# Kernel tuning notes

Measured on AMD Instinct MI355X. Metric: run time of the kernel, lower is better.

## Reference

```python
import jax, jax.numpy as jnp
import numpy as np

DT_RANK = 160
D_STATE = 16


def setup_inputs() -> dict:
    key = jax.random.key(0)
    ks = jax.random.split(key, 13)
    B, D, E = 32, 2560, 5120
    s = lambda k, shape, sc=0.02: (jax.random.normal(k, shape, dtype=jnp.float32) * sc)
    return {
        "x": jax.random.normal(ks[0], (1, 1, B, D), dtype=jnp.float32),
        "W_in_ssm": s(ks[1], (D, E)),
        "W_in_mlp": s(ks[2], (D, E)),
        "W_out": s(ks[3], (E, D)),
        "conv_w": s(ks[4], (4, B, E), 0.1),
        "conv_b": s(ks[5], (B, E), 0.1),
        "conv_states": jax.random.normal(ks[6], (3, 1, 1, B, E), dtype=jnp.float32),
        "Wx": s(ks[7], (E, DT_RANK + 2 * D_STATE)),
        "W_dt": s(ks[8], (DT_RANK, E)),
        "dt_bias": s(ks[9], (E,), 0.5),
        "A_log": jax.random.uniform(ks[10], (E, D_STATE), dtype=jnp.float32),
        "D": s(ks[11], (E,), 1.0),
        "h": jax.random.normal(ks[12], (B, E, D_STATE), dtype=jnp.float32) * 0.1,
    }


def reference(x, W_in_ssm, W_in_mlp, W_out, conv_w, conv_b, conv_states, Wx, W_dt, dt_bias, A_log, D, h):
    # x: [1,1,B,d_model]
    x_ssm = x @ W_in_ssm  # [1,1,B,E]
    # FIFO: 3 carried conv states + newest projection -> 4 taps
    states = jnp.concatenate([conv_states, x_ssm[None]], axis=0)  # [4,1,1,B,E]
    # unrolled 4-tap causal depthwise conv (per-batch-broadcast weights) + bias + SiLU
    conv = jnp.einsum('tabne,tne->abne', states, conv_w) + conv_b  # [1,1,B,E]
    conv = jax.nn.silu(conv)

    # --- single-step selective SSM (Mamba decode) ---
    xt = conv[0, 0]  # [B,E]
    dbc = xt @ Wx  # [B, dt_rank + 2*d_state]
    dt = jax.nn.softplus(dbc[:, :DT_RANK] @ W_dt + dt_bias)  # [B,E]
    Bm = dbc[:, DT_RANK:DT_RANK + D_STATE]  # [B,N]
    Cm = dbc[:, DT_RANK + D_STATE:]         # [B,N]
    A = -jnp.exp(A_log)                      # [E,N]
    dA = jnp.exp(dt[:, :, None] * A[None])   # [B,E,N]
    h_new = h * dA + (dt[:, :, None] * Bm[:, None, :]) * xt[:, :, None]
    y = jnp.einsum('ben,bn->be', h_new, Cm) + D * xt  # [B,E]
    y = y[None, None]  # [1,1,B,E]

    # gated residual branch: silu-activated mlp projection
    residual = jax.nn.silu(x @ W_in_mlp)  # [1,1,B,E]
    out = y * residual
    return out @ W_out  # [1,1,B,d_model]
```

## Files before the change

kernel.cpp:

```cpp
#include <hip/hip_runtime.h>
#include <math.h>

#define EE 5120
#define DD 2560
#define BB 32

typedef __attribute__((ext_vector_type(8)))  short  short8;
typedef __attribute__((ext_vector_type(8)))  __bf16 bf16x8;
typedef __attribute__((ext_vector_type(16))) float  f32x16;

__device__ __forceinline__ void split8(const float* v, short8& hi, short8& lo) {
#pragma unroll
  for (int j = 0; j < 8; ++j) {
    unsigned u = __float_as_uint(v[j]);
    hi[j] = (short)(u >> 16);
    float r = v[j] - __uint_as_float(u & 0xFFFF0000u);
    lo[j] = (short)(__float_as_uint(r) >> 16);
  }
}
#define BC(x) __builtin_bit_cast(bf16x8, x)

__device__ __forceinline__ void g2l16(const float* g, float* l) {
  __builtin_amdgcn_global_load_lds(
      (const __attribute__((address_space(1))) void*)g,
      (__attribute__((address_space(3))) void*)l, 16, 0, 0);
}

__global__ __launch_bounds__(256) void k0_prep(const float* __restrict__ x,
                                               float* __restrict__ xT,
                                               float* __restrict__ dbc) {
  int g = blockIdx.x * 256 + threadIdx.x;
  if (g < BB * DD) {
    int b = g / DD, k = g % DD;
    xT[k * BB + b] = x[g];
  }
  if (g < BB * 192) dbc[g] = 0.f;
}

__global__ __launch_bounds__(256) void gemm_mfma(const float* __restrict__ W0,
                                                 const float* __restrict__ W1,
                                                 int wsplit, int wstride,
                                                 const float* __restrict__ xsrc,
                                                 float* __restrict__ P,
                                                 int pstride, int ncb) {
  __shared__ float red[4 * 64 * 17];
  const int cb   = blockIdx.x % ncb;
  const int so   = blockIdx.x / ncb;
  const int lane = threadIdx.x & 63;
  const int wv   = __builtin_amdgcn_readfirstlane((int)(threadIdx.x >> 6));
  const int c0   = cb * 64;
  const float* __restrict__ W = (c0 < wsplit) ? W0 : W1;
  const int wc0  = (c0 < wsplit) ? c0 : c0 - wsplit;
  const int kw   = so * 320 + wv * 80;
  const int kl   = (lane >> 5) * 8;
  const int ln   = lane & 31;

  float av[5][8];
#pragma unroll
  for (int s = 0; s < 5; ++s)
#pragma unroll
    for (int j = 0; j < 8; ++j)
      av[s][j] = xsrc[(size_t)(kw + s * 16 + kl + j) * BB + ln];
  short8 ah[5], al[5];
#pragma unroll
  for (int s = 0; s < 5; ++s) split8(av[s], ah[s], al[s]);

#pragma unroll
  for (int t = 0; t < 2; ++t) {
    f32x16 acc;
#pragma unroll
    for (int i = 0; i < 16; ++i) acc[i] = 0.f;

    const float* __restrict__ wp =
        W + (size_t)kw * wstride + wc0 + t * 32 + ln;

    float bv0[8], bv1[8];
#pragma unroll
    for (int j = 0; j < 8; ++j) bv0[j] = wp[(size_t)(kl + j) * wstride];
#pragma unroll
    for (int s = 0; s < 5; ++s) {
      float (&cur)[8] = (s & 1) ? bv1 : bv0;
      float (&nxt)[8] = (s & 1) ? bv0 : bv1;
      if (s < 4) {
#pragma unroll
        for (int j = 0; j < 8; ++j)
          nxt[j] = wp[(size_t)((s + 1) * 16 + kl + j) * wstride];
      }
      short8 bh, bl;
      split8(cur, bh, bl);
      acc = __builtin_amdgcn_mfma_f32_32x32x16_bf16(BC(ah[s]), BC(bh), acc, 0, 0, 0);
      acc = __builtin_amdgcn_mfma_f32_32x32x16_bf16(BC(al[s]), BC(bh), acc, 0, 0, 0);
      acc = __builtin_amdgcn_mfma_f32_32x32x16_bf16(BC(ah[s]), BC(bl), acc, 0, 0, 0);
    }

    __syncthreads();
#pragma unroll
    for (int r = 0; r < 16; ++r) red[(wv * 64 + lane) * 17 + r] = acc[r];
    __syncthreads();
#pragma unroll
    for (int q = 0; q < 4; ++q) {
      int r = wv * 4 + q;
      float sum = red[(0 * 64 + lane) * 17 + r] + red[(1 * 64 + lane) * 17 + r] +
                  red[(2 * 64 + lane) * 17 + r] + red[(3 * 64 + lane) * 17 + r];
      int row = (r & 3) + 8 * (r >> 2) + 4 * (lane >> 5);
      P[((size_t)(so * 32 + row)) * pstride + c0 + t * 32 + ln] = sum;
    }
  }
}

__global__ __launch_bounds__(256) void k1b_epilogue(const float* __restrict__ P1,
                                                    const float* __restrict__ cs,
                                                    const float* __restrict__ cw,
                                                    const float* __restrict__ cbv,
                                                    float* __restrict__ xt,
                                                    float* __restrict__ res) {
  int g = blockIdx.x * 256 + threadIdx.x;
  int e = g % EE;
  int b = g / EE;
  float xs = 0.f, xm = 0.f;
#pragma unroll
  for (int so = 0; so < 8; ++so) {
    xs += P1[((size_t)(so * BB + b)) * 10240 + e];
    xm += P1[((size_t)(so * BB + b)) * 10240 + EE + e];
  }
  size_t be = (size_t)b * EE + e;
  const size_t T = (size_t)BB * EE;
  float conv = cs[be] * cw[be] + cs[T + be] * cw[T + be] +
               cs[2 * T + be] * cw[2 * T + be] + xs * cw[3 * T + be] + cbv[be];
  float sig = 1.f / (1.f + expf(-conv));
  xt[be] = conv * sig;
  float sm = 1.f / (1.f + expf(-xm));
  res[be] = xm * sm;
}

__global__ __launch_bounds__(256) void k2_dbc(const float* __restrict__ xt,
                                              const float* __restrict__ Wx,
                                              float* __restrict__ dbc) {
  const int bid  = blockIdx.x;
  const int cbi  = bid % 3;
  const int so   = bid / 3;
  const int lane = threadIdx.x & 63;
  const int j    = cbi * 64 + lane;
  const int k0   = so * 80 + (int)(threadIdx.x >> 6) * 20;

  float acc[BB];
#pragma unroll
  for (int b = 0; b < BB; ++b) acc[b] = 0.f;

  for (int kk = 0; kk < 20; kk += 4) {
    int k = k0 + kk;
    float w0 = Wx[(size_t)(k + 0) * 192 + j];
    float w1 = Wx[(size_t)(k + 1) * 192 + j];
    float w2 = Wx[(size_t)(k + 2) * 192 + j];
    float w3 = Wx[(size_t)(k + 3) * 192 + j];
#pragma unroll
    for (int b = 0; b < BB; ++b) acc[b] = fmaf(xt[(size_t)b * EE + k + 0], w0, acc[b]);
#pragma unroll
    for (int b = 0; b < BB; ++b) acc[b] = fmaf(xt[(size_t)b * EE + k + 1], w1, acc[b]);
#pragma unroll
    for (int b = 0; b < BB; ++b) acc[b] = fmaf(xt[(size_t)b * EE + k + 2], w2, acc[b]);
#pragma unroll
    for (int b = 0; b < BB; ++b) acc[b] = fmaf(xt[(size_t)b * EE + k + 3], w3, acc[b]);
  }

  __shared__ float red2[4][64][17];
  const int ksid = threadIdx.x >> 6;
#pragma unroll
  for (int half = 0; half < 2; ++half) {
    __syncthreads();
#pragma unroll
    for (int i = 0; i < 16; ++i) red2[ksid][lane][i] = acc[half * 16 + i];
    __syncthreads();
#pragma unroll
    for (int jj = 0; jj < 4; ++jj) {
      int bi = ksid * 4 + jj;
      float v = red2[0][lane][bi] + red2[1][lane][bi] +
                red2[2][lane][bi] + red2[3][lane][bi];
      int b = half * 16 + bi;
      atomicAdd(&dbc[b * 192 + j], v);
    }
  }
}

__global__ __launch_bounds__(256) void k3_ssm(const float* __restrict__ dbc,
                                              const float* __restrict__ Wdt,
                                              const float* __restrict__ dt_bias,
                                              const float* __restrict__ A_log,
                                              const float* __restrict__ Dvec,
                                              const float* __restrict__ h,
                                              const float* __restrict__ xt,
                                              const float* __restrict__ res,
                                              float* __restrict__ zT) {
  __shared__ float sw[10240];
  const int eb   = blockIdx.x % 80;
  const int bg   = blockIdx.x / 80;
  const int lane = threadIdx.x & 63;
  const int wv   = __builtin_amdgcn_readfirstlane((int)(threadIdx.x >> 6));
  const int e    = eb * 64 + lane;
  const int bq   = bg * 4 + wv;
  const int b0   = bq * 2, b1 = b0 + 1;

  {
    const int rg = lane >> 4, cg = (lane & 15) * 4;
#pragma unroll
    for (int j = 0; j < 10; ++j) {
      int r = wv * 40 + j * 4 + rg;
      g2l16(Wdt + (size_t)r * EE + eb * 64 + cg, sw + (wv * 40 + j * 4) * 64);
    }
  }
  __syncthreads();

  float a0 = 0.f, a1 = 0.f;
  const float* __restrict__ d0 = dbc + b0 * 192;
  const float* __restrict__ d1 = dbc + b1 * 192;
#pragma unroll 4
  for (int r = 0; r < 160; ++r) {
    float w = sw[r * 64 + lane];
    a0 = fmaf(d0[r], w, a0);
    a1 = fmaf(d1[r], w, a1);
  }

  float An[16];
#pragma unroll
  for (int n = 0; n < 16; ++n) An[n] = -expf(A_log[e * 16 + n]);
  const float bias = dt_bias[e];
  const float Dv = Dvec[e];

#pragma unroll
  for (int t = 0; t < 2; ++t) {
    int b = t ? b1 : b0;
    float a = t ? a1 : a0;
    float v = a + bias;
    float dt = (v > 20.f) ? v : log1pf(expf(v));
    size_t be = (size_t)b * EE + e;
    float xb = xt[be];
    const float* __restrict__ hb = h + be * 16;
    const float* __restrict__ Bm = dbc + b * 192 + 160;
    const float* __restrict__ Cm = dbc + b * 192 + 176;
    float y = 0.f;
#pragma unroll
    for (int n = 0; n < 16; ++n) {
      float dA = expf(dt * An[n]);
      float hn = fmaf(hb[n], dA, dt * Bm[n] * xb);
      y = fmaf(hn, Cm[n], y);
    }
    y = fmaf(Dv, xb, y);
    zT[e * BB + b] = y * res[be];
  }
}

__global__ __launch_bounds__(256) void k4b_reduce(const float* __restrict__ P4,
                                                  float* __restrict__ out) {
  int g = blockIdx.x * 256 + threadIdx.x;
  int d = g % DD;
  int b = g / DD;
  float s = 0.f;
#pragma unroll
  for (int so = 0; so < 16; ++so) s += P4[((size_t)(so * BB + b)) * DD + d];
  out[g] = s;
}

extern "C" void kernel_launch(void* const* d_in, const int* in_sizes, int n_in,
                              void* d_out, int out_size, void* d_ws, size_t ws_size,
                              hipStream_t stream) {
  const float* x       = (const float*)d_in[0];
  const float* Wssm    = (const float*)d_in[1];
  const float* Wmlp    = (const float*)d_in[2];
  const float* Wout    = (const float*)d_in[3];
  const float* conv_w  = (const float*)d_in[4];
  const float* conv_b  = (const float*)d_in[5];
  const float* conv_st = (const float*)d_in[6];
  const float* Wx      = (const float*)d_in[7];
  const float* Wdt     = (const float*)d_in[8];
  const float* dt_bias = (const float*)d_in[9];
  const float* A_log   = (const float*)d_in[10];
  const float* Dvec    = (const float*)d_in[11];
  const float* h       = (const float*)d_in[12];
  float* out = (float*)d_out;

  float* ws = (float*)d_ws;
  float* xT  = ws;
  float* P1  = xT  + 81920;
  float* xt  = P1  + 2621440;
  float* res = xt  + 163840;
  float* dbc = res + 163840;
  float* zT  = dbc + 6144;
  float* P4  = zT  + 163840;

  hipLaunchKernelGGL(k0_prep,     dim3(320),  dim3(256), 0, stream, x, xT, dbc);
  hipLaunchKernelGGL(gemm_mfma,   dim3(1280), dim3(256), 0, stream,
                     Wssm, Wmlp, EE, EE, xT, P1, 10240, 160);
  hipLaunchKernelGGL(k1b_epilogue,dim3(640),  dim3(256), 0, stream, P1, conv_st, conv_w, conv_b, xt, res);
  hipLaunchKernelGGL(k2_dbc,      dim3(192),  dim3(256), 0, stream, xt, Wx, dbc);
  hipLaunchKernelGGL(k3_ssm,      dim3(320),  dim3(256), 0, stream, dbc, Wdt, dt_bias, A_log, Dvec, h, xt, res, zT);
  hipLaunchKernelGGL(gemm_mfma,   dim3(640),  dim3(256), 0, stream,
                     Wout, Wout, 1 << 30, DD, zT, P4, DD, 40);
  hipLaunchKernelGGL(k4b_reduce,  dim3(320),  dim3(256), 0, stream, P4, out);
}
```

Before: 249.5 us.

## Use single-wave GEMM blocks over full K-slab; fuse output reduction via atomics

```diff
diff --git a/kernel.cpp b/kernel.cpp
--- a/kernel.cpp
+++ b/kernel.cpp
@@ -37,73 +37,70 @@
   if (g < BB * 192) dbc[g] = 0.f;
 }
 
-__global__ __launch_bounds__(256) void gemm_mfma(const float* __restrict__ W0,
-                                                 const float* __restrict__ W1,
-                                                 int wsplit, int wstride,
-                                                 const float* __restrict__ xsrc,
-                                                 float* __restrict__ P,
-                                                 int pstride, int ncb) {
-  __shared__ float red[4 * 64 * 17];
+__global__ __launch_bounds__(64) void gemm_mfma(const float* __restrict__ W0,
+                                                const float* __restrict__ W1,
+                                                int wsplit, int wstride,
+                                                const float* __restrict__ xsrc,
+                                                float* __restrict__ P,
+                                                int pstride, int ncb,
+                                                int atomic) {
   const int cb   = blockIdx.x % ncb;
   const int so   = blockIdx.x / ncb;
   const int lane = threadIdx.x & 63;
-  const int wv   = __builtin_amdgcn_readfirstlane((int)(threadIdx.x >> 6));
-  const int c0   = cb * 64;
+  const int c0   = cb * 32;
   const float* __restrict__ W = (c0 < wsplit) ? W0 : W1;
   const int wc0  = (c0 < wsplit) ? c0 : c0 - wsplit;
-  const int kw   = so * 320 + wv * 80;
+  const int kw   = so * 320;
   const int kl   = (lane >> 5) * 8;
   const int ln   = lane & 31;
 
-  float av[5][8];
-#pragma unroll
-  for (int s = 0; s < 5; ++s)
-#pragma unroll
-    for (int j = 0; j < 8; ++j)
-      av[s][j] = xsrc[(size_t)(kw + s * 16 + kl + j) * BB + ln];
-  short8 ah[5], al[5];
-#pragma unroll
-  for (int s = 0; s < 5; ++s) split8(av[s], ah[s], al[s]);
-
-#pragma unroll
-  for (int t = 0; t < 2; ++t) {
-    f32x16 acc;
-#pragma unroll
-    for (int i = 0; i < 16; ++i) acc[i] = 0.f;
-
-    const float* __restrict__ wp =
-        W + (size_t)kw * wstride + wc0 + t * 32 + ln;
-
-    float bv0[8], bv1[8];
-#pragma unroll
-    for (int j = 0; j < 8; ++j) bv0[j] = wp[(size_t)(kl + j) * wstride];
-#pragma unroll
-    for (int s = 0; s < 5; ++s) {
-      float (&cur)[8] = (s & 1) ? bv1 : bv0;
-      float (&nxt)[8] = (s & 1) ? bv0 : bv1;
-      if (s < 4) {
-#pragma unroll
-        for (int j = 0; j < 8; ++j)
-          nxt[j] = wp[(size_t)((s + 1) * 16 + kl + j) * wstride];
+  const float* __restrict__ ap = xsrc + (size_t)(kw + kl) * BB + ln;
+  const float* __restrict__ wp = W + (size_t)(kw + kl) * wstride + wc0 + ln;
+
+  float ab[4][8], bb[4][8];
+#pragma unroll
+  for (int p = 0; p < 3; ++p) {
+#pragma unroll
+    for (int j = 0; j < 8; ++j) {
+      ab[p][j] = ap[(size_t)(p * 16 + j) * BB];
+      bb[p][j] = wp[(size_t)(p * 16 + j) * wstride];
+    }
+  }
+
+  f32x16 acc;
+#pragma unroll
+  for (int i = 0; i < 16; ++i) acc[i] = 0.f;
+
+#pragma unroll
+  for (int s = 0; s < 20; ++s) {
+    if (s < 17) {
+      const int pn = (s + 3) & 3;
+#pragma unroll
+      for (int j = 0; j < 8; ++j) {
+        ab[pn][j] = ap[(size_t)((s + 3) * 16 + j) * BB];
+        bb[pn][j] = wp[(size_t)((s + 3) * 16 + j) * wstride];
       }
-      short8 bh, bl;
-      split8(cur, bh, bl);
-      acc = __builtin_amdgcn_mfma_f32_32x32x16_bf16(BC(ah[s]), BC(bh), acc, 0, 0, 0);
-      acc = __builtin_amdgcn_mfma_f32_32x32x16_bf16(BC(al[s]), BC(bh), acc, 0, 0, 0);
-      acc = __builtin_amdgcn_mfma_f32_32x32x16_bf16(BC(ah[s]), BC(bl), acc, 0, 0, 0);
-    }
-
-    __syncthreads();
-#pragma unroll
-    for (int r = 0; r < 16; ++r) red[(wv * 64 + lane) * 17 + r] = acc[r];
-    __syncthreads();
-#pragma unroll
-    for (int q = 0; q < 4; ++q) {
-      int r = wv * 4 + q;
-      float sum = red[(0 * 64 + lane) * 17 + r] + red[(1 * 64 + lane) * 17 + r] +
-                  red[(2 * 64 + lane) * 17 + r] + red[(3 * 64 + lane) * 17 + r];
+    }
+    const int pc = s & 3;
+    short8 ah, al, bh, bl;
+    split8(ab[pc], ah, al);
+    split8(bb[pc], bh, bl);
+    acc = __builtin_amdgcn_mfma_f32_32x32x16_bf16(BC(ah), BC(bh), acc, 0, 0, 0);
+    acc = __builtin_amdgcn_mfma_f32_32x32x16_bf16(BC(al), BC(bh), acc, 0, 0, 0);
+    acc = __builtin_amdgcn_mfma_f32_32x32x16_bf16(BC(ah), BC(bl), acc, 0, 0, 0);
+  }
+
+  if (atomic) {
+#pragma unroll
+    for (int r = 0; r < 16; ++r) {
       int row = (r & 3) + 8 * (r >> 2) + 4 * (lane >> 5);
-      P[((size_t)(so * 32 + row)) * pstride + c0 + t * 32 + ln] = sum;
+      atomicAdd(&P[(size_t)row * pstride + c0 + ln], acc[r]);
+    }
+  } else {
+#pragma unroll
+    for (int r = 0; r < 16; ++r) {
+      int row = (r & 3) + 8 * (r >> 2) + 4 * (lane >> 5);
+      P[((size_t)(so * 32 + row)) * pstride + c0 + ln] = acc[r];
     }
   }
 }
@@ -190,7 +187,8 @@
                                               const float* __restrict__ h,
                                               const float* __restrict__ xt,
                                               const float* __restrict__ res,
-                                              float* __restrict__ zT) {
+                                              float* __restrict__ zT,
+                                              float* __restrict__ out) {
   __shared__ float sw[10240];
   const int eb   = blockIdx.x % 80;
   const int bg   = blockIdx.x / 80;
@@ -199,6 +197,8 @@
   const int e    = eb * 64 + lane;
   const int bq   = bg * 4 + wv;
   const int b0   = bq * 2, b1 = b0 + 1;
+
+  out[blockIdx.x * 256 + threadIdx.x] = 0.f;
 
   {
     const int rg = lane >> 4, cg = (lane & 15) * 4;
@@ -247,17 +247,6 @@
     y = fmaf(Dv, xb, y);
     zT[e * BB + b] = y * res[be];
   }
-}
-
-__global__ __launch_bounds__(256) void k4b_reduce(const float* __restrict__ P4,
-                                                  float* __restrict__ out) {
-  int g = blockIdx.x * 256 + threadIdx.x;
-  int d = g % DD;
-  int b = g / DD;
-  float s = 0.f;
-#pragma unroll
-  for (int so = 0; so < 16; ++so) s += P4[((size_t)(so * BB + b)) * DD + d];
-  out[g] = s;
 }
 
 extern "C" void kernel_launch(void* const* d_in, const int* in_sizes, int n_in,
@@ -285,15 +274,13 @@
   float* res = xt  + 163840;
   float* dbc = res + 163840;
   float* zT  = dbc + 6144;
-  float* P4  = zT  + 163840;
 
   hipLaunchKernelGGL(k0_prep,     dim3(320),  dim3(256), 0, stream, x, xT, dbc);
-  hipLaunchKernelGGL(gemm_mfma,   dim3(1280), dim3(256), 0, stream,
-                     Wssm, Wmlp, EE, EE, xT, P1, 10240, 160);
+  hipLaunchKernelGGL(gemm_mfma,   dim3(2560), dim3(64),  0, stream,
+                     Wssm, Wmlp, EE, EE, xT, P1, 10240, 320, 0);
   hipLaunchKernelGGL(k1b_epilogue,dim3(640),  dim3(256), 0, stream, P1, conv_st, conv_w, conv_b, xt, res);
   hipLaunchKernelGGL(k2_dbc,      dim3(192),  dim3(256), 0, stream, xt, Wx, dbc);
-  hipLaunchKernelGGL(k3_ssm,      dim3(320),  dim3(256), 0, stream, dbc, Wdt, dt_bias, A_log, Dvec, h, xt, res, zT);
-  hipLaunchKernelGGL(gemm_mfma,   dim3(640),  dim3(256), 0, stream,
-                     Wout, Wout, 1 << 30, DD, zT, P4, DD, 40);
-  hipLaunchKernelGGL(k4b_reduce,  dim3(320),  dim3(256), 0, stream, P4, out);
-}
+  hipLaunchKernelGGL(k3_ssm,      dim3(320),  dim3(256), 0, stream, dbc, Wdt, dt_bias, A_log, Dvec, h, xt, res, zT, out);
+  hipLaunchKernelGGL(gemm_mfma,   dim3(1280), dim3(64),  0, stream,
+                     Wout, Wout, 1 << 30, DD, zT, out, DD, 80, 1);
+}
```

Result: no change. 249.5 us (+0.0%).
